# Kernel optimization log

Measured on AMD Instinct MI355X. Metric: run time of the kernel, lower is better.

## Reference

```python
import jax, jax.numpy as jnp
import numpy as np

N = 50000        # num nodes
E = 800000       # num edges (avg degree 16)
NFEAT = 128
NHID = 128
NCLASS = 64


def setup_inputs() -> dict:
    key = jax.random.key(0)
    k0, k1, k2, k3 = jax.random.split(key, 4)
    x = jax.random.normal(k0, (N, NFEAT), dtype=jnp.float32)
    edge_index = jax.random.randint(k1, (2, E), 0, N)
    edge_weight = jnp.ones((E,), dtype=jnp.float32)
    # GCNConv linear weights (glorot-ish uniform), biases zero
    s1 = 1.0 / np.sqrt(NFEAT)
    W1 = jax.random.uniform(k2, (NFEAT, NHID), jnp.float32, -s1, s1)
    b1 = jnp.zeros((NHID,), jnp.float32)
    s2 = 1.0 / np.sqrt(NHID)
    W2 = jax.random.uniform(k3, (NHID, NCLASS), jnp.float32, -s2, s2)
    b2 = jnp.zeros((NCLASS,), jnp.float32)
    return {"x": x, "edge_index": edge_index, "edge_weight": edge_weight,
            "W1": W1, "b1": b1, "W2": W2, "b2": b2}


def reference(x, edge_index, edge_weight, W1, b1, W2, b2):
    n = x.shape[0]
    # add self loops (fill_value = 1.0), as GCNConv(add_self_loops=True)
    loops = jnp.arange(n)
    ei = jnp.concatenate([edge_index, jnp.stack([loops, loops])], axis=1)
    ew = jnp.concatenate([edge_weight, jnp.ones((n,), x.dtype)])
    row, col = ei[0], ei[1]
    # symmetric gcn normalization: D^-1/2 A D^-1/2
    deg = jax.ops.segment_sum(ew, col, num_segments=n)
    dinv = jnp.where(deg > 0, jax.lax.rsqrt(deg), 0.0)
    norm = dinv[row] * ew * dinv[col]        # [E+N]

    def conv(h, W, b):
        h = h @ W                                   # [N, F_out]
        msg = norm[:, None] * h[row]                # gather + scale, [E+N, F_out]
        return jax.ops.segment_sum(msg, col, num_segments=n) + b

    h = jax.nn.relu(conv(x, W1, b1))  # dropout p=0.0 -> identity
    out = conv(h, W2, b2)
    # F.normalize(p=2, dim=-1)
    nrm = jnp.linalg.norm(out, axis=-1, keepdims=True)
    return out / jnp.maximum(nrm, 1e-12)
```

## Files before the change

### kernel.cpp

```cpp
#include <hip/hip_runtime.h>

#define NF 128
#define NC 64

__device__ __forceinline__ unsigned f2bf(float f) {
    unsigned u = __float_as_uint(f);
    return (u + 0x7FFFu + ((u >> 16) & 1u)) >> 16;
}
__device__ __forceinline__ float bf2f(unsigned h) { return __uint_as_float(h << 16); }

__global__ __launch_bounds__(256) void gemm1_cnt_fused(const float* __restrict__ X,
                                                       const float* __restrict__ W,
                                                       unsigned short* __restrict__ H,
                                                       const int* __restrict__ col,
                                                       int* __restrict__ cnt,
                                                       int* __restrict__ eoff,
                                                       int N, int E, int CB) {
    __shared__ float Xs[32][128];
    __shared__ float Wsh[32][128];
    if ((int)blockIdx.x < CB) {
        int stride = CB * 256;
        for (int e = blockIdx.x * 256 + threadIdx.x; e < E; e += stride)
            eoff[e] = atomicAdd(&cnt[col[e]], 1);
        return;
    }
    const int bm0 = (blockIdx.x - CB) * 128;
    const int tid = threadIdx.x;
    const int tx = tid & 15, ty = tid >> 4;
    float acc[2][2][4][4] = {};
    for (int kc = 0; kc < 4; ++kc) {
        {
            int r = tid >> 1;
            int k0 = (tid & 1) * 16;
            int node = min(bm0 + r, N - 1);
            const float4* src = (const float4*)(X + (size_t)node * 128 + kc * 32 + k0);
#pragma unroll
            for (int j4 = 0; j4 < 4; ++j4) {
                float4 v = src[j4];
                int k = k0 + j4 * 4;
                Xs[k + 0][r] = v.x;
                Xs[k + 1][r] = v.y;
                Xs[k + 2][r] = v.z;
                Xs[k + 3][r] = v.w;
            }
        }
        {
            const float4* src = (const float4*)(W + (size_t)kc * 32 * 128);
            float4* dst = (float4*)&Wsh[0][0];
#pragma unroll
            for (int i = tid; i < 32 * 128 / 4; i += 256) dst[i] = src[i];
        }
        __syncthreads();
#pragma unroll 4
        for (int k = 0; k < 32; ++k) {
            float4 xa = *(const float4*)&Xs[k][tx * 4];
            float4 xb = *(const float4*)&Xs[k][64 + tx * 4];
            float xv[2][4] = {{xa.x, xa.y, xa.z, xa.w}, {xb.x, xb.y, xb.z, xb.w}};
            float wv[2][4];
#pragma unroll
            for (int c = 0; c < 2; ++c) {
                float4 w4 = *(const float4*)&Wsh[k][c * 64 + ty * 4];
                wv[c][0] = w4.x; wv[c][1] = w4.y; wv[c][2] = w4.z; wv[c][3] = w4.w;
            }
#pragma unroll
            for (int h = 0; h < 2; ++h)
#pragma unroll
                for (int c = 0; c < 2; ++c)
#pragma unroll
                    for (int i = 0; i < 4; ++i)
#pragma unroll
                        for (int j = 0; j < 4; ++j)
                            acc[h][c][i][j] = fmaf(xv[h][i], wv[c][j], acc[h][c][i][j]);
        }
        __syncthreads();
    }
#pragma unroll
    for (int h = 0; h < 2; ++h)
#pragma unroll
        for (int i = 0; i < 4; ++i) {
            int n = bm0 + h * 64 + tx * 4 + i;
            if (n < N) {
#pragma unroll
                for (int c = 0; c < 2; ++c) {
                    ushort4 o;
                    o.x = (unsigned short)f2bf(acc[h][c][i][0]);
                    o.y = (unsigned short)f2bf(acc[h][c][i][1]);
                    o.z = (unsigned short)f2bf(acc[h][c][i][2]);
                    o.w = (unsigned short)f2bf(acc[h][c][i][3]);
                    *(ushort4*)&H[(size_t)n * 128 + c * 64 + ty * 4] = o;
                }
            }
        }
}

__global__ __launch_bounds__(256) void scan_blocks(const int* __restrict__ cnt,
                                                   int* __restrict__ excl,
                                                   int* __restrict__ bsum, int N) {
    __shared__ int sh[256];
    int t = threadIdx.x;
    int base = blockIdx.x * 1024 + t * 4;
    int v0 = base + 0 < N ? cnt[base + 0] : 0;
    int v1 = base + 1 < N ? cnt[base + 1] : 0;
    int v2 = base + 2 < N ? cnt[base + 2] : 0;
    int v3 = base + 3 < N ? cnt[base + 3] : 0;
    int s = v0 + v1 + v2 + v3;
    sh[t] = s;
    __syncthreads();
    for (int off = 1; off < 256; off <<= 1) {
        int x = (t >= off) ? sh[t - off] : 0;
        __syncthreads();
        sh[t] += x;
        __syncthreads();
    }
    int incl = sh[t];
    int exclT = incl - s;
    if (t == 255) bsum[blockIdx.x] = incl;
    if (base + 0 < N) excl[base + 0] = exclT;
    if (base + 1 < N) excl[base + 1] = exclT + v0;
    if (base + 2 < N) excl[base + 2] = exclT + v0 + v1;
    if (base + 3 < N) excl[base + 3] = exclT + v0 + v1 + v2;
}

__global__ void scan_sums(int* __restrict__ bsum, int nb) {
    int run = 0;
    for (int i = 0; i < nb; ++i) { int v = bsum[i]; bsum[i] = run; run += v; }
    bsum[nb] = run;
}

__global__ __launch_bounds__(256) void scan_add(int* __restrict__ excl,
                                                const int* __restrict__ bsum,
                                                int N, int nb) {
    int i = blockIdx.x * 256 + threadIdx.x;
    if (i < N) excl[i] += bsum[i >> 10];
    if (i == 0) excl[N] = bsum[nb];
}

__global__ __launch_bounds__(256) void scatter_kernel(const int* __restrict__ row,
                                                      const int* __restrict__ col,
                                                      const float* __restrict__ ew,
                                                      const int* __restrict__ rowPtr,
                                                      const int* __restrict__ eoff,
                                                      int2* __restrict__ csr, int E) {
    int e = blockIdx.x * 256 + threadIdx.x;
    if (e >= E) return;
    int c = col[e];
    csr[rowPtr[c] + eoff[e]] = make_int2(row[e], __float_as_int(ew[e]));
}

__global__ __launch_bounds__(256) void deg_dinv_kernel(const int* __restrict__ rowPtr,
                                                       const int2* __restrict__ csr,
                                                       float* __restrict__ dinv, int N) {
    int idx = blockIdx.x * 256 + threadIdx.x;
    int n = idx >> 4, l = idx & 15;
    if (n >= N) return;
    int beg = rowPtr[n], end = rowPtr[n + 1];
    float s = 0.f;
    for (int i = beg + l; i < end; i += 16) s += __int_as_float(csr[i].y);
#pragma unroll
    for (int off = 8; off; off >>= 1) s += __shfl_xor(s, off, 16);
    if (l == 0) dinv[n] = rsqrtf(s + 1.0f);
}

__global__ __launch_bounds__(256) void norm_csr_kernel(int2* __restrict__ csr,
                                                       const float* __restrict__ dinv, int E) {
    int i = blockIdx.x * 256 + threadIdx.x;
    if (i >= E) return;
    int2 p = csr[i];
    ((int*)csr)[2 * i + 1] = __float_as_int(__int_as_float(p.y) * dinv[p.x]);
}

__global__ __launch_bounds__(256) void agg_gather1(const int* __restrict__ rowPtr,
                                                   const int2* __restrict__ csr,
                                                   const unsigned* __restrict__ H1u,
                                                   const float* __restrict__ dinv,
                                                   const float2* __restrict__ b2,
                                                   float2* __restrict__ out2, int N) {
    int n = (blockIdx.x * 256 + threadIdx.x) >> 6;
    int lane = threadIdx.x & 63;
    if (n >= N) return;
    float dn = dinv[n];
    float accx = 0.f, accy = 0.f;
    int beg = rowPtr[n], end = rowPtr[n + 1];
    int j = beg;
    for (; j + 4 <= end; j += 4) {
        int2 p0 = csr[j + 0], p1 = csr[j + 1], p2 = csr[j + 2], p3 = csr[j + 3];
        unsigned v0 = H1u[(size_t)p0.x * 64 + lane];
        unsigned v1 = H1u[(size_t)p1.x * 64 + lane];
        unsigned v2 = H1u[(size_t)p2.x * 64 + lane];
        unsigned v3 = H1u[(size_t)p3.x * 64 + lane];
        float w0 = __int_as_float(p0.y), w1 = __int_as_float(p1.y);
        float w2 = __int_as_float(p2.y), w3 = __int_as_float(p3.y);
        accx += w0 * bf2f(v0 & 0xffffu); accy += w0 * bf2f(v0 >> 16);
        accx += w1 * bf2f(v1 & 0xffffu); accy += w1 * bf2f(v1 >> 16);
        accx += w2 * bf2f(v2 & 0xffffu); accy += w2 * bf2f(v2 >> 16);
        accx += w3 * bf2f(v3 & 0xffffu); accy += w3 * bf2f(v3 >> 16);
    }
    for (; j < end; ++j) {
        int2 p = csr[j];
        unsigned v = H1u[(size_t)p.x * 64 + lane];
        float w = __int_as_float(p.y);
        accx += w * bf2f(v & 0xffffu); accy += w * bf2f(v >> 16);
    }
    unsigned hv = H1u[(size_t)n * 64 + lane];
    float2 bb = b2[lane];
    float s = dn * dn;
    float2 o;
    o.x = fmaxf(fmaf(dn, accx, s * bf2f(hv & 0xffffu)) + bb.x, 0.f);
    o.y = fmaxf(fmaf(dn, accy, s * bf2f(hv >> 16)) + bb.y, 0.f);
    out2[(size_t)n * 64 + lane] = o;
}

__global__ __launch_bounds__(256) void gemm_tile64(const float* __restrict__ X,
                                                   const float* __restrict__ W,
                                                   unsigned short* __restrict__ H, int N) {
    __shared__ float Xs[32][128];
    __shared__ float Wsh[32][64];
    const int bm0 = blockIdx.x * 128;
    const int tid = threadIdx.x;
    const int tx = tid & 15, ty = tid >> 4;
    float acc[2][4][4] = {};
    for (int kc = 0; kc < 4; ++kc) {
        {
            int r = tid >> 1;
            int k0 = (tid & 1) * 16;
            int node = min(bm0 + r, N - 1);
            const float4* src = (const float4*)(X + (size_t)node * 128 + kc * 32 + k0);
#pragma unroll
            for (int j4 = 0; j4 < 4; ++j4) {
                float4 v = src[j4];
                int k = k0 + j4 * 4;
                Xs[k + 0][r] = v.x;
                Xs[k + 1][r] = v.y;
                Xs[k + 2][r] = v.z;
                Xs[k + 3][r] = v.w;
            }
        }
        {
            const float4* src = (const float4*)(W + (size_t)kc * 32 * 64);
            float4* dst = (float4*)&Wsh[0][0];
#pragma unroll
            for (int i = tid; i < 32 * 64 / 4; i += 256) dst[i] = src[i];
        }
        __syncthreads();
#pragma unroll 4
        for (int k = 0; k < 32; ++k) {
            float4 xa = *(const float4*)&Xs[k][tx * 4];
            float4 xb = *(const float4*)&Xs[k][64 + tx * 4];
            float xv[2][4] = {{xa.x, xa.y, xa.z, xa.w}, {xb.x, xb.y, xb.z, xb.w}};
            float4 w4 = *(const float4*)&Wsh[k][ty * 4];
            float wv[4] = {w4.x, w4.y, w4.z, w4.w};
#pragma unroll
            for (int h = 0; h < 2; ++h)
#pragma unroll
                for (int i = 0; i < 4; ++i)
#pragma unroll
                    for (int j = 0; j < 4; ++j)
                        acc[h][i][j] = fmaf(xv[h][i], wv[j], acc[h][i][j]);
        }
        __syncthreads();
    }
#pragma unroll
    for (int h = 0; h < 2; ++h)
#pragma unroll
        for (int i = 0; i < 4; ++i) {
            int n = bm0 + h * 64 + tx * 4 + i;
            if (n < N) {
                ushort4 o;
                o.x = (unsigned short)f2bf(acc[h][i][0]);
                o.y = (unsigned short)f2bf(acc[h][i][1]);
                o.z = (unsigned short)f2bf(acc[h][i][2]);
                o.w = (unsigned short)f2bf(acc[h][i][3]);
                *(ushort4*)&H[(size_t)n * 64 + ty * 4] = o;
            }
        }
}

__global__ __launch_bounds__(256) void agg_gather2(const int* __restrict__ rowPtr,
                                                   const int2* __restrict__ csr,
                                                   const unsigned* __restrict__ H3u,
                                                   const float* __restrict__ dinv,
                                                   const float2* __restrict__ b2,
                                                   float2* __restrict__ out2, int N) {
    int n = (blockIdx.x * 256 + threadIdx.x) >> 5;
    int l = threadIdx.x & 31;
    if (n >= N) return;
    float dn = dinv[n];
    float accx = 0.f, accy = 0.f;
    int beg = rowPtr[n], end = rowPtr[n + 1];
    int j = beg;
    for (; j + 4 <= end; j += 4) {
        int2 p0 = csr[j + 0], p1 = csr[j + 1], p2 = csr[j + 2], p3 = csr[j + 3];
        unsigned v0 = H3u[(size_t)p0.x * 32 + l];
        unsigned v1 = H3u[(size_t)p1.x * 32 + l];
        unsigned v2 = H3u[(size_t)p2.x * 32 + l];
        unsigned v3 = H3u[(size_t)p3.x * 32 + l];
        float w0 = __int_as_float(p0.y), w1 = __int_as_float(p1.y);
        float w2 = __int_as_float(p2.y), w3 = __int_as_float(p3.y);
        accx += w0 * bf2f(v0 & 0xffffu); accy += w0 * bf2f(v0 >> 16);
        accx += w1 * bf2f(v1 & 0xffffu); accy += w1 * bf2f(v1 >> 16);
        accx += w2 * bf2f(v2 & 0xffffu); accy += w2 * bf2f(v2 >> 16);
        accx += w3 * bf2f(v3 & 0xffffu); accy += w3 * bf2f(v3 >> 16);
    }
    for (; j < end; ++j) {
        int2 p = csr[j];
        unsigned v = H3u[(size_t)p.x * 32 + l];
        float w = __int_as_float(p.y);
        accx += w * bf2f(v & 0xffffu); accy += w * bf2f(v >> 16);
    }
    unsigned hv = H3u[(size_t)n * 32 + l];
    float2 bb = b2[l];
    float s = dn * dn;
    float vx = fmaf(dn, accx, s * bf2f(hv & 0xffffu)) + bb.x;
    float vy = fmaf(dn, accy, s * bf2f(hv >> 16)) + bb.y;
    float ss = vx * vx + vy * vy;
#pragma unroll
    for (int off = 16; off; off >>= 1) ss += __shfl_xor(ss, off, 64);
    float scale = 1.0f / fmaxf(sqrtf(ss), 1e-12f);
    out2[(size_t)n * 32 + l] = make_float2(vx * scale, vy * scale);
}

extern "C" void kernel_launch(void* const* d_in, const int* in_sizes, int n_in,
                              void* d_out, int out_size, void* d_ws, size_t ws_size,
                              hipStream_t stream) {
    const float* x  = (const float*)d_in[0];
    const int*   ei = (const int*)d_in[1];
    const float* ew = (const float*)d_in[2];
    const float* W1 = (const float*)d_in[3];
    const float* b1 = (const float*)d_in[4];
    const float* W2 = (const float*)d_in[5];
    const float* b2 = (const float*)d_in[6];
    float* out = (float*)d_out;
    const int N = in_sizes[0] / NF;
    const int E = in_sizes[2];
    const int* row = ei;
    const int* col = ei + E;
    const int NB = (N + 1023) / 1024;

    char* ws = (char*)d_ws;
    size_t off = 0;
    auto take = [&](size_t bytes) {
        char* p = ws + off;
        off = (off + bytes + 255) & ~(size_t)255;
        return p;
    };
    float* dinv   = (float*)take((size_t)N * 4);
    int*   cnt    = (int*)  take((size_t)N * 4);
    int*   rowPtr = (int*)  take((size_t)(N + 1) * 4);
    int*   eoff   = (int*)  take((size_t)E * 4);
    int*   bsum   = (int*)  take((size_t)(NB + 1) * 4);
    int2*  csr    = (int2*) take((size_t)E * 8);
    unsigned short* H1 = (unsigned short*)take((size_t)N * NF * 2);
    float* buf2   = (float*)take((size_t)N * NF * 4);
    unsigned short* H3 = (unsigned short*)take((size_t)N * NC * 2);

    hipMemsetAsync(cnt, 0, (size_t)N * 4, stream);

    const int CB = 256;
    const int GB = (N + 127) / 128;
    gemm1_cnt_fused<<<CB + GB, 256, 0, stream>>>(x, W1, H1, col, cnt, eoff, N, E, CB);

    scan_blocks<<<NB, 256, 0, stream>>>(cnt, rowPtr, bsum, N);
    scan_sums<<<1, 1, 0, stream>>>(bsum, NB);
    scan_add<<<(N + 255) / 256, 256, 0, stream>>>(rowPtr, bsum, N, NB);
    scatter_kernel<<<(E + 255) / 256, 256, 0, stream>>>(row, col, ew, rowPtr, eoff, csr, E);

    deg_dinv_kernel<<<(N * 16 + 255) / 256, 256, 0, stream>>>(rowPtr, csr, dinv, N);
    norm_csr_kernel<<<(E + 255) / 256, 256, 0, stream>>>(csr, dinv, E);

    agg_gather1<<<(N * 64 + 255) / 256, 256, 0, stream>>>(rowPtr, csr, (const unsigned*)H1,
                                                          dinv, (const float2*)b1,
                                                          (float2*)buf2, N);

    gemm_tile64<<<(N + 127) / 128, 256, 0, stream>>>(buf2, W2, H3, N);
    agg_gather2<<<(N * 32 + 255) / 256, 256, 0, stream>>>(rowPtr, csr, (const unsigned*)H3,
                                                          dinv, (const float2*)b2,
                                                          (float2*)out, N);
}
```

Baseline: 175.1 us.

## Replace global-atomic CSR counting with sliced LDS histograms and fuse scatter with GEMM1

Edge counting now runs as per-slice, per-half-node-range shared-memory histograms with packed 16-bit counters, instead of global atomics. A per-node scan over 64 slices produces slice offsets, which removes the memset and the global atomic contention. The scatter is fused with the first GEMM, and both GEMMs move to 64-row tiles for more blocks. H3 reuses the H1 buffer. The costs are extra passes over col (two halves times 64 slices), a 64×N ushort offset table, and a strided scan with poorly coalesced accesses.

```diff
diff --git a/kernel.cpp b/kernel.cpp
--- a/kernel.cpp
+++ b/kernel.cpp
@@ -2,6 +2,7 @@
 
 #define NF 128
 #define NC 64
+#define SLICES 64
 
 __device__ __forceinline__ unsigned f2bf(float f) {
     unsigned u = __float_as_uint(f);
@@ -9,88 +10,46 @@
 }
 __device__ __forceinline__ float bf2f(unsigned h) { return __uint_as_float(h << 16); }
 
-__global__ __launch_bounds__(256) void gemm1_cnt_fused(const float* __restrict__ X,
-                                                       const float* __restrict__ W,
-                                                       unsigned short* __restrict__ H,
-                                                       const int* __restrict__ col,
-                                                       int* __restrict__ cnt,
-                                                       int* __restrict__ eoff,
-                                                       int N, int E, int CB) {
-    __shared__ float Xs[32][128];
-    __shared__ float Wsh[32][128];
-    if ((int)blockIdx.x < CB) {
-        int stride = CB * 256;
-        for (int e = blockIdx.x * 256 + threadIdx.x; e < E; e += stride)
-            eoff[e] = atomicAdd(&cnt[col[e]], 1);
-        return;
-    }
-    const int bm0 = (blockIdx.x - CB) * 128;
-    const int tid = threadIdx.x;
-    const int tx = tid & 15, ty = tid >> 4;
-    float acc[2][2][4][4] = {};
-    for (int kc = 0; kc < 4; ++kc) {
-        {
-            int r = tid >> 1;
-            int k0 = (tid & 1) * 16;
-            int node = min(bm0 + r, N - 1);
-            const float4* src = (const float4*)(X + (size_t)node * 128 + kc * 32 + k0);
-#pragma unroll
-            for (int j4 = 0; j4 < 4; ++j4) {
-                float4 v = src[j4];
-                int k = k0 + j4 * 4;
-                Xs[k + 0][r] = v.x;
-                Xs[k + 1][r] = v.y;
-                Xs[k + 2][r] = v.z;
-                Xs[k + 3][r] = v.w;
-            }
-        }
-        {
-            const float4* src = (const float4*)(W + (size_t)kc * 32 * 128);
-            float4* dst = (float4*)&Wsh[0][0];
-#pragma unroll
-            for (int i = tid; i < 32 * 128 / 4; i += 256) dst[i] = src[i];
-        }
-        __syncthreads();
+__global__ __launch_bounds__(256) void count_rank_kernel(const int* __restrict__ col,
+                                                         unsigned short* __restrict__ eoff16,
+                                                         unsigned short* __restrict__ C16,
+                                                         int N, int E, int SL, int nh) {
+    __shared__ unsigned hist[12544];
+    const int j = blockIdx.x >> 1;
+    const int h = blockIdx.x & 1;
+    const int nlo = h * nh;
+    const int nhi = min(N, nlo + nh);
+    const int words = (nhi - nlo + 1) >> 1;
+    for (int i = threadIdx.x; i < words; i += 256) hist[i] = 0;
+    __syncthreads();
+    const int e0 = j * SL, e1 = min(E, e0 + SL);
+    for (int e = e0 + threadIdx.x; e < e1; e += 256) {
+        int c = col[e];
+        if (c >= nlo && c < nhi) {
+            int cl = c - nlo;
+            unsigned sh = (cl & 1) * 16;
+            unsigned old = atomicAdd(&hist[cl >> 1], 1u << sh);
+            eoff16[e] = (unsigned short)((old >> sh) & 0xffffu);
+        }
+    }
+    __syncthreads();
+    unsigned* Cw = (unsigned*)(C16 + (size_t)j * N + nlo);
+    for (int i = threadIdx.x; i < words; i += 256) Cw[i] = hist[i];
+}
+
+__global__ __launch_bounds__(256) void scanC_kernel(unsigned short* __restrict__ C16,
+                                                    int* __restrict__ tot, int N) {
+    int n = blockIdx.x * 256 + threadIdx.x;
+    if (n >= N) return;
+    int t = 0;
 #pragma unroll 4
-        for (int k = 0; k < 32; ++k) {
-            float4 xa = *(const float4*)&Xs[k][tx * 4];
-            float4 xb = *(const float4*)&Xs[k][64 + tx * 4];
-            float xv[2][4] = {{xa.x, xa.y, xa.z, xa.w}, {xb.x, xb.y, xb.z, xb.w}};
-            float wv[2][4];
-#pragma unroll
-            for (int c = 0; c < 2; ++c) {
-                float4 w4 = *(const float4*)&Wsh[k][c * 64 + ty * 4];
-                wv[c][0] = w4.x; wv[c][1] = w4.y; wv[c][2] = w4.z; wv[c][3] = w4.w;
-            }
-#pragma unroll
-            for (int h = 0; h < 2; ++h)
-#pragma unroll
-                for (int c = 0; c < 2; ++c)
-#pragma unroll
-                    for (int i = 0; i < 4; ++i)
-#pragma unroll
-                        for (int j = 0; j < 4; ++j)
-                            acc[h][c][i][j] = fmaf(xv[h][i], wv[c][j], acc[h][c][i][j]);
-        }
-        __syncthreads();
-    }
-#pragma unroll
-    for (int h = 0; h < 2; ++h)
-#pragma unroll
-        for (int i = 0; i < 4; ++i) {
-            int n = bm0 + h * 64 + tx * 4 + i;
-            if (n < N) {
-#pragma unroll
-                for (int c = 0; c < 2; ++c) {
-                    ushort4 o;
-                    o.x = (unsigned short)f2bf(acc[h][c][i][0]);
-                    o.y = (unsigned short)f2bf(acc[h][c][i][1]);
-                    o.z = (unsigned short)f2bf(acc[h][c][i][2]);
-                    o.w = (unsigned short)f2bf(acc[h][c][i][3]);
-                    *(ushort4*)&H[(size_t)n * 128 + c * 64 + ty * 4] = o;
-                }
-            }
-        }
+    for (int j = 0; j < SLICES; ++j) {
+        size_t idx = (size_t)j * N + n;
+        int v = C16[idx];
+        C16[idx] = (unsigned short)t;
+        t += v;
+    }
+    tot[n] = t;
 }
 
 __global__ __launch_bounds__(256) void scan_blocks(const int* __restrict__ cnt,
@@ -135,16 +94,83 @@
     if (i == 0) excl[N] = bsum[nb];
 }
 
-__global__ __launch_bounds__(256) void scatter_kernel(const int* __restrict__ row,
-                                                      const int* __restrict__ col,
-                                                      const float* __restrict__ ew,
-                                                      const int* __restrict__ rowPtr,
-                                                      const int* __restrict__ eoff,
-                                                      int2* __restrict__ csr, int E) {
-    int e = blockIdx.x * 256 + threadIdx.x;
-    if (e >= E) return;
-    int c = col[e];
-    csr[rowPtr[c] + eoff[e]] = make_int2(row[e], __float_as_int(ew[e]));
+__global__ __launch_bounds__(256) void scatter_gemm1_fused(const int* __restrict__ row,
+                                                           const int* __restrict__ col,
+                                                           const float* __restrict__ ew,
+                                                           const int* __restrict__ rowPtr,
+                                                           const unsigned short* __restrict__ Coff16,
+                                                           const unsigned short* __restrict__ eoff16,
+                                                           int2* __restrict__ csr,
+                                                           const float* __restrict__ X,
+                                                           const float* __restrict__ W,
+                                                           unsigned short* __restrict__ H,
+                                                           int N, int E, int SL, int SB) {
+    __shared__ float Xs[32][64];
+    __shared__ float Wsh[32][128];
+    if ((int)blockIdx.x < SB) {
+        int stride = SB * 256;
+        for (int e = blockIdx.x * 256 + threadIdx.x; e < E; e += stride) {
+            int c = col[e];
+            int j = e / SL;
+            int idx = rowPtr[c] + (int)Coff16[(size_t)j * N + c] + (int)eoff16[e];
+            csr[idx] = make_int2(row[e], __float_as_int(ew[e]));
+        }
+        return;
+    }
+    const int bm0 = (blockIdx.x - SB) * 64;
+    const int tid = threadIdx.x;
+    const int tx = tid & 15, ty = tid >> 4;
+    float acc[4][8] = {};
+    for (int kc = 0; kc < 4; ++kc) {
+        {
+            int r = tid >> 2, q = tid & 3;
+            int node = min(bm0 + r, N - 1);
+            const float4* src = (const float4*)(X + (size_t)node * 128 + kc * 32);
+#pragma unroll
+            for (int qq = 0; qq < 2; ++qq) {
+                float4 v = src[q + qq * 4];
+                int k = (q + qq * 4) * 4;
+                Xs[k + 0][r] = v.x;
+                Xs[k + 1][r] = v.y;
+                Xs[k + 2][r] = v.z;
+                Xs[k + 3][r] = v.w;
+            }
+        }
+        {
+            const float4* src = (const float4*)(W + (size_t)kc * 32 * 128);
+            float4* dst = (float4*)&Wsh[0][0];
+#pragma unroll
+            for (int i = tid; i < 1024; i += 256) dst[i] = src[i];
+        }
+        __syncthreads();
+#pragma unroll 4
+        for (int k = 0; k < 32; ++k) {
+            float4 xa = *(const float4*)&Xs[k][tx * 4];
+            float4 wA = *(const float4*)&Wsh[k][ty * 8];
+            float4 wB = *(const float4*)&Wsh[k][ty * 8 + 4];
+            float xv[4] = {xa.x, xa.y, xa.z, xa.w};
+            float wv[8] = {wA.x, wA.y, wA.z, wA.w, wB.x, wB.y, wB.z, wB.w};
+#pragma unroll
+            for (int i = 0; i < 4; ++i)
+#pragma unroll
+                for (int j = 0; j < 8; ++j)
+                    acc[i][j] = fmaf(xv[i], wv[j], acc[i][j]);
+        }
+        __syncthreads();
+    }
+#pragma unroll
+    for (int i = 0; i < 4; ++i) {
+        int n = bm0 + tx * 4 + i;
+        if (n < N) {
+            ushort4 oA, oB;
+            oA.x = (unsigned short)f2bf(acc[i][0]); oA.y = (unsigned short)f2bf(acc[i][1]);
+            oA.z = (unsigned short)f2bf(acc[i][2]); oA.w = (unsigned short)f2bf(acc[i][3]);
+            oB.x = (unsigned short)f2bf(acc[i][4]); oB.y = (unsigned short)f2bf(acc[i][5]);
+            oB.z = (unsigned short)f2bf(acc[i][6]); oB.w = (unsigned short)f2bf(acc[i][7]);
+            *(ushort4*)&H[(size_t)n * 128 + ty * 8] = oA;
+            *(ushort4*)&H[(size_t)n * 128 + ty * 8 + 4] = oB;
+        }
+    }
 }
 
 __global__ __launch_bounds__(256) void deg_dinv_kernel(const int* __restrict__ rowPtr,
@@ -213,22 +239,21 @@
 __global__ __launch_bounds__(256) void gemm_tile64(const float* __restrict__ X,
                                                    const float* __restrict__ W,
                                                    unsigned short* __restrict__ H, int N) {
-    __shared__ float Xs[32][128];
+    __shared__ float Xs[32][64];
     __shared__ float Wsh[32][64];
-    const int bm0 = blockIdx.x * 128;
+    const int bm0 = blockIdx.x * 64;
     const int tid = threadIdx.x;
     const int tx = tid & 15, ty = tid >> 4;
-    float acc[2][4][4] = {};
+    float acc[4][4] = {};
     for (int kc = 0; kc < 4; ++kc) {
         {
-            int r = tid >> 1;
-            int k0 = (tid & 1) * 16;
+            int r = tid >> 2, q = tid & 3;
             int node = min(bm0 + r, N - 1);
-            const float4* src = (const float4*)(X + (size_t)node * 128 + kc * 32 + k0);
-#pragma unroll
-            for (int j4 = 0; j4 < 4; ++j4) {
-                float4 v = src[j4];
-                int k = k0 + j4 * 4;
+            const float4* src = (const float4*)(X + (size_t)node * 128 + kc * 32);
+#pragma unroll
+            for (int qq = 0; qq < 2; ++qq) {
+                float4 v = src[q + qq * 4];
+                int k = (q + qq * 4) * 4;
                 Xs[k + 0][r] = v.x;
                 Xs[k + 1][r] = v.y;
                 Xs[k + 2][r] = v.z;
@@ -239,40 +264,35 @@
             const float4* src = (const float4*)(W + (size_t)kc * 32 * 64);
             float4* dst = (float4*)&Wsh[0][0];
 #pragma unroll
-            for (int i = tid; i < 32 * 64 / 4; i += 256) dst[i] = src[i];
+            for (int i = tid; i < 512; i += 256) dst[i] = src[i];
         }
         __syncthreads();
 #pragma unroll 4
         for (int k = 0; k < 32; ++k) {
             float4 xa = *(const float4*)&Xs[k][tx * 4];
-            float4 xb = *(const float4*)&Xs[k][64 + tx * 4];
-            float xv[2][4] = {{xa.x, xa.y, xa.z, xa.w}, {xb.x, xb.y, xb.z, xb.w}};
             float4 w4 = *(const float4*)&Wsh[k][ty * 4];
+            float xv[4] = {xa.x, xa.y, xa.z, xa.w};
             float wv[4] = {w4.x, w4.y, w4.z, w4.w};
 #pragma unroll
-            for (int h = 0; h < 2; ++h)
-#pragma unroll
-                for (int i = 0; i < 4; ++i)
-#pragma unroll
-                    for (int j = 0; j < 4; ++j)
-                        acc[h][i][j] = fmaf(xv[h][i], wv[j], acc[h][i][j]);
-        }
-        __syncthreads();
-    }
-#pragma unroll
-    for (int h = 0; h < 2; ++h)
-#pragma unroll
-        for (int i = 0; i < 4; ++i) {
-            int n = bm0 + h * 64 + tx * 4 + i;
-            if (n < N) {
-                ushort4 o;
-                o.x = (unsigned short)f2bf(acc[h][i][0]);
-                o.y = (unsigned short)f2bf(acc[h][i][1]);
-                o.z = (unsigned short)f2bf(acc[h][i][2]);
-                o.w = (unsigned short)f2bf(acc[h][i][3]);
-                *(ushort4*)&H[(size_t)n * 64 + ty * 4] = o;
-            }
-        }
+            for (int i = 0; i < 4; ++i)
+#pragma unroll
+                for (int j = 0; j < 4; ++j)
+                    acc[i][j] = fmaf(xv[i], wv[j], acc[i][j]);
+        }
+        __syncthreads();
+    }
+#pragma unroll
+    for (int i = 0; i < 4; ++i) {
+        int n = bm0 + tx * 4 + i;
+        if (n < N) {
+            ushort4 o;
+            o.x = (unsigned short)f2bf(acc[i][0]);
+            o.y = (unsigned short)f2bf(acc[i][1]);
+            o.z = (unsigned short)f2bf(acc[i][2]);
+            o.w = (unsigned short)f2bf(acc[i][3]);
+            *(ushort4*)&H[(size_t)n * 64 + ty * 4] = o;
+        }
+    }
 }
 
 __global__ __launch_bounds__(256) void agg_gather2(const int* __restrict__ rowPtr,
@@ -335,6 +355,8 @@
     const int* row = ei;
     const int* col = ei + E;
     const int NB = (N + 1023) / 1024;
+    const int SL = (E + SLICES - 1) / SLICES;
+    const int nh = (N + 1) / 2;
 
     char* ws = (char*)d_ws;
     size_t off = 0;
@@ -344,25 +366,26 @@
         return p;
     };
     float* dinv   = (float*)take((size_t)N * 4);
-    int*   cnt    = (int*)  take((size_t)N * 4);
+    int*   tot    = (int*)  take((size_t)N * 4);
     int*   rowPtr = (int*)  take((size_t)(N + 1) * 4);
-    int*   eoff   = (int*)  take((size_t)E * 4);
+    unsigned short* eoff16 = (unsigned short*)take((size_t)E * 2);
     int*   bsum   = (int*)  take((size_t)(NB + 1) * 4);
+    unsigned short* C16    = (unsigned short*)take((size_t)SLICES * N * 2);
     int2*  csr    = (int2*) take((size_t)E * 8);
     unsigned short* H1 = (unsigned short*)take((size_t)N * NF * 2);
     float* buf2   = (float*)take((size_t)N * NF * 4);
-    unsigned short* H3 = (unsigned short*)take((size_t)N * NC * 2);
-
-    hipMemsetAsync(cnt, 0, (size_t)N * 4, stream);
-
-    const int CB = 256;
-    const int GB = (N + 127) / 128;
-    gemm1_cnt_fused<<<CB + GB, 256, 0, stream>>>(x, W1, H1, col, cnt, eoff, N, E, CB);
-
-    scan_blocks<<<NB, 256, 0, stream>>>(cnt, rowPtr, bsum, N);
+    unsigned short* H3 = H1;
+
+    count_rank_kernel<<<2 * SLICES, 256, 0, stream>>>(col, eoff16, C16, N, E, SL, nh);
+    scanC_kernel<<<(N + 255) / 256, 256, 0, stream>>>(C16, tot, N);
+    scan_blocks<<<NB, 256, 0, stream>>>(tot, rowPtr, bsum, N);
     scan_sums<<<1, 1, 0, stream>>>(bsum, NB);
     scan_add<<<(N + 255) / 256, 256, 0, stream>>>(rowPtr, bsum, N, NB);
-    scatter_kernel<<<(E + 255) / 256, 256, 0, stream>>>(row, col, ew, rowPtr, eoff, csr, E);
+
+    const int SB = 128;
+    const int GB = (N + 63) / 64;
+    scatter_gemm1_fused<<<SB + GB, 256, 0, stream>>>(row, col, ew, rowPtr, C16, eoff16,
+                                                     csr, x, W1, H1, N, E, SL, SB);
 
     deg_dinv_kernel<<<(N * 16 + 255) / 256, 256, 0, stream>>>(rowPtr, csr, dinv, N);
     norm_csr_kernel<<<(E + 255) / 256, 256, 0, stream>>>(csr, dinv, E);
@@ -371,7 +394,7 @@
                                                           dinv, (const float2*)b1,
                                                           (float2*)buf2, N);
 
-    gemm_tile64<<<(N + 127) / 128, 256, 0, stream>>>(buf2, W2, H3, N);
+    gemm_tile64<<<(N + 63) / 64, 256, 0, stream>>>(buf2, W2, H3, N);
     agg_gather2<<<(N * 32 + 255) / 256, 256, 0, stream>>>(rowPtr, csr, (const unsigned*)H3,
                                                           dinv, (const float2*)b2,
                                                           (float2*)out, N);
```

New measurement: 174.4 us. About the same (-0.4%).
